# Kernel optimization log

Hardware: AMD Instinct MI355X
Metric: run time of the kernel (lower is better)

The kernel has to match this reference:

```python
import jax, jax.numpy as jnp
import numpy as np

EMBED = 768
HEADS = 12
HEAD_DIM = EMBED // HEADS
B, S = 2, 2048


def setup_inputs() -> dict:
    key = jax.random.key(0)
    ks = jax.random.split(key, 5)
    scale = 1.0 / np.sqrt(EMBED)
    return {
        "x": jax.random.normal(ks[0], (B, S, EMBED), dtype=jnp.float32),
        "w_q": jax.random.normal(ks[1], (EMBED, EMBED), dtype=jnp.float32) * scale,
        "b_q": jnp.zeros((EMBED,), dtype=jnp.float32),
        "w_k": jax.random.normal(ks[2], (EMBED, EMBED), dtype=jnp.float32) * scale,
        "b_k": jnp.zeros((EMBED,), dtype=jnp.float32),
        "w_v": jax.random.normal(ks[3], (EMBED, EMBED), dtype=jnp.float32) * scale,
        "b_v": jnp.zeros((EMBED,), dtype=jnp.float32),
        "w_o": jax.random.normal(ks[4], (EMBED, EMBED), dtype=jnp.float32) * scale,
        "b_o": jnp.zeros((EMBED,), dtype=jnp.float32),
    }


def reference(x, w_q, b_q, w_k, b_k, w_v, b_v, w_o, b_o):
    b, s, _ = x.shape
    # QKV projections (torch Linear: y = x @ W^T + b)
    q = x @ w_q.T + b_q
    k = x @ w_k.T + b_k
    v = x @ w_v.T + b_v
    # split heads -> [b, h, s, d]
    def split(t):
        return t.reshape(b, s, HEADS, HEAD_DIM).transpose(0, 2, 1, 3)
    q, k, v = split(q), split(k), split(v)
    scores = jnp.einsum("bhqd,bhkd->bhqk", q, k) / jnp.sqrt(
        jnp.asarray(HEAD_DIM, dtype=jnp.float32))
    probs = jax.nn.softmax(scores, axis=-1)
    out = jnp.einsum("bhqk,bhkd->bhqd", probs, v)
    out = out.transpose(0, 2, 1, 3).reshape(b, s, EMBED)
    return out @ w_o.T + b_o
```

## Files before the change

kernel.cpp:

```cpp
#include <hip/hip_runtime.h>
#include <math.h>

#define EMBED 768
#define HEADS 12
#define HDIM 64
#define BATCH 2
#define SEQ 2048
#define MTOT (BATCH*SEQ)

typedef short s8v __attribute__((ext_vector_type(8)));
typedef short s4v __attribute__((ext_vector_type(4)));
typedef float f4v __attribute__((ext_vector_type(4)));

__device__ __forceinline__ short f2bf(float f) {
    union { float f; unsigned u; } v; v.f = f;
    unsigned r = v.u + 0x7FFFu + ((v.u >> 16) & 1u);
    return (short)(r >> 16);
}

__device__ __forceinline__ unsigned pk2bf(float a, float b) {
    union { float f; unsigned u; } x, y; x.f = a; y.f = b;
    return ((y.u + 0x8000u) & 0xFFFF0000u) | ((x.u + 0x8000u) >> 16);
}

__device__ __forceinline__ unsigned cvtpk(float a, float b) {
    unsigned r;
    asm("v_cvt_pk_bf16_f32 %0, %1, %2" : "=v"(r) : "v"(a), "v"(b));
    return r;
}

__device__ __forceinline__ float fexp2(float x) {
#if __has_builtin(__builtin_amdgcn_exp2f)
    return __builtin_amdgcn_exp2f(x);
#else
    return exp2f(x);
#endif
}

__device__ __forceinline__ void gll16(const short* g, short* l) {
    __builtin_amdgcn_global_load_lds((const __attribute__((address_space(1))) void*)g,
                                     (__attribute__((address_space(3))) void*)l, 16, 0, 0);
}

__global__ __launch_bounds__(256) void cvt_all(
        const float* __restrict__ x,  const float* __restrict__ wq,
        const float* __restrict__ wk, const float* __restrict__ wv,
        const float* __restrict__ wo,
        short* __restrict__ xb, short* __restrict__ wqb, short* __restrict__ wkb,
        short* __restrict__ wvb, short* __restrict__ wob) {
    const int seg = blockIdx.y;
    const float* src; short* dst; int n4;
    if      (seg == 0) { src = x;  dst = xb;  n4 = MTOT * EMBED / 4; }
    else if (seg == 1) { src = wq; dst = wqb; n4 = EMBED * EMBED / 4; }
    else if (seg == 2) { src = wk; dst = wkb; n4 = EMBED * EMBED / 4; }
    else if (seg == 3) { src = wv; dst = wvb; n4 = EMBED * EMBED / 4; }
    else               { src = wo; dst = wob; n4 = EMBED * EMBED / 4; }
    for (int i = blockIdx.x * 256 + threadIdx.x; i < n4; i += gridDim.x * 256) {
        float4 f = ((const float4*)src)[i];
        short4 o;
        o.x = f2bf(f.x); o.y = f2bf(f.y); o.z = f2bf(f.z); o.w = f2bf(f.w);
        ((short4*)dst)[i] = o;
    }
}

__global__ __launch_bounds__(256, 4) void gemm_qkv(const short* __restrict__ A,
        const short* __restrict__ Wq, const short* __restrict__ Wk, const short* __restrict__ Wv,
        const float* __restrict__ bq, const float* __restrict__ bk, const float* __restrict__ bv,
        short* __restrict__ Qo, short* __restrict__ Ko, short* __restrict__ Vo) {
    const int mode = blockIdx.z;
    const short* W    = (mode == 0) ? Wq : (mode == 1) ? Wk : Wv;
    const float* bias = (mode == 0) ? bq : (mode == 1) ? bk : bv;
    const float qs = (mode == 0) ? (0.125f * 1.44269504f) : 1.0f;

    __shared__ short As[128 * 32];
    __shared__ short Ws[128 * 32];

    const int tid = threadIdx.x;
    const int lane = tid & 63, wid = tid >> 6;
    const int quad = lane >> 4, lr = lane & 15;
    const int m0 = blockIdx.x * 128, n0 = blockIdx.y * 128;
    const int wm = (wid >> 1) * 64, wn = (wid & 1) * 64;
    const int ar = lane >> 2, ac = (lane & 3) * 8;

    f4v acc[4][4];
    for (int a = 0; a < 4; a++)
        for (int b = 0; b < 4; b++)
            for (int i = 0; i < 4; i++) acc[a][b][i] = 0.f;

    for (int k0 = 0; k0 < EMBED; k0 += 32) {
        gll16(&A[(long)(m0 + wid * 32 + ar) * EMBED + k0 + ac],      &As[(wid * 32) * 32]);
        gll16(&A[(long)(m0 + wid * 32 + 16 + ar) * EMBED + k0 + ac], &As[(wid * 32 + 16) * 32]);
        gll16(&W[(long)(n0 + wid * 32 + ar) * EMBED + k0 + ac],      &Ws[(wid * 32) * 32]);
        gll16(&W[(long)(n0 + wid * 32 + 16 + ar) * EMBED + k0 + ac], &Ws[(wid * 32 + 16) * 32]);
        __syncthreads();

        s8v af[4], bf[4];
        for (int mi = 0; mi < 4; mi++)
            af[mi] = *(const s8v*)&As[(wm + mi * 16 + lr) * 32 + quad * 8];
        for (int ni = 0; ni < 4; ni++)
            bf[ni] = *(const s8v*)&Ws[(wn + ni * 16 + lr) * 32 + quad * 8];
        for (int mi = 0; mi < 4; mi++)
            for (int ni = 0; ni < 4; ni++)
                acc[mi][ni] = __builtin_amdgcn_mfma_f32_16x16x32_bf16(af[mi], bf[ni], acc[mi][ni], 0, 0, 0);
        __syncthreads();
    }

    if (mode == 2) {
        for (int mi = 0; mi < 4; mi++) {
            int srow = m0 + wm + mi * 16 + quad * 4;
            int b = srow >> 11, s = srow & 2047;
            for (int ni = 0; ni < 4; ni++) {
                int n = n0 + wn + ni * 16 + lr;
                int h = n >> 6, d = n & 63;
                float bb = bias[n];
                uint2 pk;
                pk.x = pk2bf(acc[mi][ni][0] + bb, acc[mi][ni][1] + bb);
                pk.y = pk2bf(acc[mi][ni][2] + bb, acc[mi][ni][3] + bb);
                *(uint2*)&Vo[(((long)(b * HEADS + h) * HDIM + d) * SEQ) + s] = pk;
            }
        }
    } else {
        short* Out = (mode == 0) ? Qo : Ko;
        for (int mi = 0; mi < 4; mi++) {
            for (int ni = 0; ni < 4; ni++) {
                int n = n0 + wn + ni * 16 + lr;
                int h = n >> 6, d = n & 63;
                float bb = bias[n];
                for (int i = 0; i < 4; i++) {
                    int m = m0 + wm + mi * 16 + quad * 4 + i;
                    int b = m >> 11, s = m & 2047;
                    Out[(((long)(b * HEADS + h) * SEQ + s) * HDIM) + d] =
                        f2bf((acc[mi][ni][i] + bb) * qs);
                }
            }
        }
    }
}

__global__ __launch_bounds__(256, 4) void gemm_out(const short* __restrict__ A,
        const short* __restrict__ W, const float* __restrict__ bias,
        float* __restrict__ Out) {
    __shared__ short As[128 * 32];
    __shared__ short Ws[64 * 32];

    const int tid = threadIdx.x;
    const int lane = tid & 63, wid = tid >> 6;
    const int quad = lane >> 4, lr = lane & 15;
    const int m0 = blockIdx.x * 128, n0 = blockIdx.y * 64;
    const int wm = (wid >> 1) * 64, wn = (wid & 1) * 32;
    const int ar = lane >> 2, ac = (lane & 3) * 8;

    f4v acc[4][2];
    for (int a = 0; a < 4; a++)
        for (int b = 0; b < 2; b++)
            for (int i = 0; i < 4; i++) acc[a][b][i] = 0.f;

    for (int k0 = 0; k0 < EMBED; k0 += 32) {
        gll16(&A[(long)(m0 + wid * 32 + ar) * EMBED + k0 + ac],      &As[(wid * 32) * 32]);
        gll16(&A[(long)(m0 + wid * 32 + 16 + ar) * EMBED + k0 + ac], &As[(wid * 32 + 16) * 32]);
        gll16(&W[(long)(n0 + wid * 16 + ar) * EMBED + k0 + ac],      &Ws[(wid * 16) * 32]);
        __syncthreads();

        s8v af[4], bf[2];
        for (int mi = 0; mi < 4; mi++)
            af[mi] = *(const s8v*)&As[(wm + mi * 16 + lr) * 32 + quad * 8];
        for (int ni = 0; ni < 2; ni++)
            bf[ni] = *(const s8v*)&Ws[(wn + ni * 16 + lr) * 32 + quad * 8];
        for (int mi = 0; mi < 4; mi++)
            for (int ni = 0; ni < 2; ni++)
                acc[mi][ni] = __builtin_amdgcn_mfma_f32_16x16x32_bf16(af[mi], bf[ni], acc[mi][ni], 0, 0, 0);
        __syncthreads();
    }

    for (int mi = 0; mi < 4; mi++)
        for (int ni = 0; ni < 2; ni++)
            for (int i = 0; i < 4; i++) {
                int m = m0 + wm + mi * 16 + quad * 4 + i;
                int n = n0 + wn + ni * 16 + lr;
                Out[(long)m * EMBED + n] = acc[mi][ni][i] + bias[n];
            }
}

__global__ __launch_bounds__(256, 4) void flash_attn(const short* __restrict__ Q,
        const short* __restrict__ K, const short* __restrict__ Vt,
        short* __restrict__ Out) {
    extern __shared__ char pool[];
    short* Ks = (short*)pool;
    short* Vs = Ks + 2 * 64 * 64;

    const int bh = blockIdx.y;
    const int tid = threadIdx.x, lane = tid & 63, wid = tid >> 6;
    const int quad = lane >> 4, lr = lane & 15;
    const int q0 = blockIdx.x * 64;
    const int qw = q0 + wid * 16;

    const short* Qb = Q  + (long)bh * SEQ * HDIM;
    const short* Kb = K  + (long)bh * SEQ * HDIM;
    const short* Vb = Vt + (long)bh * HDIM * SEQ;

    s8v qf[2];
#pragma unroll
    for (int hh = 0; hh < 2; hh++)
        qf[hh] = *(const s8v*)&Qb[(qw + lr) * HDIM + hh * 32 + quad * 8];

    f4v o[4];
#pragma unroll
    for (int dt = 0; dt < 4; dt++)
        for (int i = 0; i < 4; i++) o[dt][i] = 0.f;
    float lsum = 0.f;

    const float SB2 = -16.0f * 1.44269504f;

    const int srow  = lane >> 3;
    const int sslot = (lane & 7) ^ srow;

#pragma unroll
    for (int i = 0; i < 2; i++) {
        const int r0 = wid * 16 + i * 8;
        gll16(&Kb[(long)(r0 + srow) * HDIM + sslot * 8], &Ks[r0 * 64]);
        gll16(&Vb[(long)(r0 + srow) * SEQ + sslot * 8], &Vs[r0 * 64]);
    }
    __syncthreads();

    for (int r = 0; r < 32; r++) {
        const int cur = r & 1;
        const short* Kc = Ks + cur * (64 * 64);
        const short* Vc = Vs + cur * (64 * 64);
        short* Kn = Ks + (cur ^ 1) * (64 * 64);
        short* Vn = Vs + (cur ^ 1) * (64 * 64);

        if (r < 31) {
            const int kn0 = (r + 1) * 64;
#pragma unroll
            for (int i = 0; i < 2; i++) {
                const int r0 = wid * 16 + i * 8;
                gll16(&Kb[(long)(kn0 + r0 + srow) * HDIM + sslot * 8], &Kn[r0 * 64]);
                gll16(&Vb[(long)(r0 + srow) * SEQ + kn0 + sslot * 8], &Vn[r0 * 64]);
            }
        }

        unsigned pw[2][4];
#pragma unroll
        for (int nt = 0; nt < 4; nt++) {
            const int row = nt * 16 + lr;
            s8v kf0 = *(const s8v*)&Kc[row * 64 + ((quad ^ (lr & 7)) * 8)];
            s8v kf1 = *(const s8v*)&Kc[row * 64 + (((4 + quad) ^ (lr & 7)) * 8)];
            f4v s = {SB2, SB2, SB2, SB2};
            s = __builtin_amdgcn_mfma_f32_16x16x32_bf16(kf0, qf[0], s, 0, 0, 0);
            s = __builtin_amdgcn_mfma_f32_16x16x32_bf16(kf1, qf[1], s, 0, 0, 0);
            float p0 = fexp2(s[0]);
            float p1 = fexp2(s[1]);
            float p2 = fexp2(s[2]);
            float p3 = fexp2(s[3]);
            lsum += (p0 + p1) + (p2 + p3);
            pw[nt >> 1][(nt & 1) * 2]     = cvtpk(p0, p1);
            pw[nt >> 1][(nt & 1) * 2 + 1] = cvtpk(p2, p3);
        }

#pragma unroll
        for (int h = 0; h < 2; h++) {
            s8v pf = *(s8v*)&pw[h][0];
            const int cb0 = h * 4 + (quad >> 1);
#pragma unroll
            for (int dt = 0; dt < 4; dt++) {
                const int d = dt * 16 + lr;
                const int c0 = cb0 ^ (lr & 7);
                const int c1 = (cb0 + 2) ^ (lr & 7);
                s4v v0 = *(const s4v*)&Vc[d * 64 + c0 * 8 + (quad & 1) * 4];
                s4v v1 = *(const s4v*)&Vc[d * 64 + c1 * 8 + (quad & 1) * 4];
                s8v vf = __builtin_shufflevector(v0, v1, 0, 1, 2, 3, 4, 5, 6, 7);
                o[dt] = __builtin_amdgcn_mfma_f32_16x16x32_bf16(pf, vf, o[dt], 0, 0, 0);
            }
        }
        __syncthreads();
    }

    lsum += __shfl_xor(lsum, 16);
    lsum += __shfl_xor(lsum, 32);
    float linv[4];
#pragma unroll
    for (int i = 0; i < 4; i++)
        linv[i] = 1.0f / __shfl(lsum, quad * 4 + i);

    const int b = bh / HEADS, h = bh % HEADS;
#pragma unroll
    for (int dt = 0; dt < 4; dt++)
#pragma unroll
        for (int i = 0; i < 4; i++) {
            const int q = qw + quad * 4 + i;
            Out[((long)(b * SEQ + q)) * EMBED + h * HDIM + dt * 16 + lr] =
                f2bf(o[dt][i] * linv[i]);
        }
}

extern "C" void kernel_launch(void* const* d_in, const int* in_sizes, int n_in,
                              void* d_out, int out_size, void* d_ws, size_t ws_size,
                              hipStream_t stream) {
    const float* x   = (const float*)d_in[0];
    const float* w_q = (const float*)d_in[1];
    const float* b_q = (const float*)d_in[2];
    const float* w_k = (const float*)d_in[3];
    const float* b_k = (const float*)d_in[4];
    const float* w_v = (const float*)d_in[5];
    const float* b_v = (const float*)d_in[6];
    const float* w_o = (const float*)d_in[7];
    const float* b_o = (const float*)d_in[8];

    short* x_bf   = (short*)d_ws;
    short* wq_bf  = x_bf  + MTOT * EMBED;
    short* wk_bf  = wq_bf + EMBED * EMBED;
    short* wv_bf  = wk_bf + EMBED * EMBED;
    short* wo_bf  = wv_bf + EMBED * EMBED;
    short* q_bf   = wo_bf + EMBED * EMBED;
    short* k_bf   = q_bf  + BATCH * HEADS * SEQ * HDIM;
    short* v_bf   = k_bf  + BATCH * HEADS * SEQ * HDIM;
    short* att_bf = v_bf  + BATCH * HEADS * SEQ * HDIM;

    cvt_all<<<dim3(1024, 5), 256, 0, stream>>>(x, w_q, w_k, w_v, w_o,
                                               x_bf, wq_bf, wk_bf, wv_bf, wo_bf);

    gemm_qkv<<<dim3(MTOT / 128, EMBED / 128, 3), 256, 0, stream>>>(
        x_bf, wq_bf, wk_bf, wv_bf, b_q, b_k, b_v, q_bf, k_bf, v_bf);

    flash_attn<<<dim3(SEQ / 64, BATCH * HEADS), 256, 32768, stream>>>(
        q_bf, k_bf, v_bf, att_bf);

    gemm_out<<<dim3(MTOT / 128, EMBED / 64), 256, 0, stream>>>(
        att_bf, wo_bf, b_o, (float*)d_out);
}
```

Measured before the change: 164.1 us.

## Widen GEMM K-tile to 64 with XOR-swizzled LDS layout

Both projection GEMMs now stage K-tiles of 64 instead of 32, which halves the number of barrier pairs per output tile. Each 64-element shared-memory row is written with an XOR swizzle on its 16-byte slots, and the MFMA fragment reads apply the same swizzle to avoid LDS bank conflicts. This doubles LDS use per block, which may limit occupancy under the four-blocks-per-CU launch bound.

```diff
diff --git a/kernel.cpp b/kernel.cpp
--- a/kernel.cpp
+++ b/kernel.cpp
@@ -72,43 +72,50 @@
     const float* bias = (mode == 0) ? bq : (mode == 1) ? bk : bv;
     const float qs = (mode == 0) ? (0.125f * 1.44269504f) : 1.0f;
 
-    __shared__ short As[128 * 32];
-    __shared__ short Ws[128 * 32];
+    __shared__ short As[128 * 64];
+    __shared__ short Ws[128 * 64];
 
     const int tid = threadIdx.x;
     const int lane = tid & 63, wid = tid >> 6;
     const int quad = lane >> 4, lr = lane & 15;
     const int m0 = blockIdx.x * 128, n0 = blockIdx.y * 128;
     const int wm = (wid >> 1) * 64, wn = (wid & 1) * 64;
-    const int ar = lane >> 2, ac = (lane & 3) * 8;
+
+    const int srow  = lane >> 3;
+    const int sslot = (lane & 7) ^ srow;
 
     f4v acc[4][4];
     for (int a = 0; a < 4; a++)
         for (int b = 0; b < 4; b++)
             for (int i = 0; i < 4; i++) acc[a][b][i] = 0.f;
 
-    for (int k0 = 0; k0 < EMBED; k0 += 32) {
-        gll16(&A[(long)(m0 + wid * 32 + ar) * EMBED + k0 + ac],      &As[(wid * 32) * 32]);
-        gll16(&A[(long)(m0 + wid * 32 + 16 + ar) * EMBED + k0 + ac], &As[(wid * 32 + 16) * 32]);
-        gll16(&W[(long)(n0 + wid * 32 + ar) * EMBED + k0 + ac],      &Ws[(wid * 32) * 32]);
-        gll16(&W[(long)(n0 + wid * 32 + 16 + ar) * EMBED + k0 + ac], &Ws[(wid * 32 + 16) * 32]);
-        __syncthreads();
-
-        s8v af[4], bf[4];
-        for (int mi = 0; mi < 4; mi++)
-            af[mi] = *(const s8v*)&As[(wm + mi * 16 + lr) * 32 + quad * 8];
-        for (int ni = 0; ni < 4; ni++)
-            bf[ni] = *(const s8v*)&Ws[(wn + ni * 16 + lr) * 32 + quad * 8];
-        for (int mi = 0; mi < 4; mi++)
+    for (int k0 = 0; k0 < EMBED; k0 += 64) {
+#pragma unroll
+        for (int i = 0; i < 4; i++) {
+            const int r0 = wid * 32 + i * 8;
+            gll16(&A[(long)(m0 + r0 + srow) * EMBED + k0 + sslot * 8], &As[r0 * 64]);
+            gll16(&W[(long)(n0 + r0 + srow) * EMBED + k0 + sslot * 8], &Ws[r0 * 64]);
+        }
+        __syncthreads();
+
+#pragma unroll
+        for (int kk = 0; kk < 2; kk++) {
+            s8v af[4], bf[4];
+            for (int mi = 0; mi < 4; mi++)
+                af[mi] = *(const s8v*)&As[(wm + mi * 16 + lr) * 64 + (((kk * 4 + quad) ^ (lr & 7)) * 8)];
             for (int ni = 0; ni < 4; ni++)
-                acc[mi][ni] = __builtin_amdgcn_mfma_f32_16x16x32_bf16(af[mi], bf[ni], acc[mi][ni], 0, 0, 0);
+                bf[ni] = *(const s8v*)&Ws[(wn + ni * 16 + lr) * 64 + (((kk * 4 + quad) ^ (lr & 7)) * 8)];
+            for (int mi = 0; mi < 4; mi++)
+                for (int ni = 0; ni < 4; ni++)
+                    acc[mi][ni] = __builtin_amdgcn_mfma_f32_16x16x32_bf16(af[mi], bf[ni], acc[mi][ni], 0, 0, 0);
+        }
         __syncthreads();
     }
 
     if (mode == 2) {
         for (int mi = 0; mi < 4; mi++) {
-            int srow = m0 + wm + mi * 16 + quad * 4;
-            int b = srow >> 11, s = srow & 2047;
+            int srow2 = m0 + wm + mi * 16 + quad * 4;
+            int b = srow2 >> 11, s = srow2 & 2047;
             for (int ni = 0; ni < 4; ni++) {
                 int n = n0 + wn + ni * 16 + lr;
                 int h = n >> 6, d = n & 63;
@@ -140,35 +147,47 @@
 __global__ __launch_bounds__(256, 4) void gemm_out(const short* __restrict__ A,
         const short* __restrict__ W, const float* __restrict__ bias,
         float* __restrict__ Out) {
-    __shared__ short As[128 * 32];
-    __shared__ short Ws[64 * 32];
+    __shared__ short As[128 * 64];
+    __shared__ short Ws[64 * 64];
 
     const int tid = threadIdx.x;
     const int lane = tid & 63, wid = tid >> 6;
     const int quad = lane >> 4, lr = lane & 15;
     const int m0 = blockIdx.x * 128, n0 = blockIdx.y * 64;
     const int wm = (wid >> 1) * 64, wn = (wid & 1) * 32;
-    const int ar = lane >> 2, ac = (lane & 3) * 8;
+
+    const int srow  = lane >> 3;
+    const int sslot = (lane & 7) ^ srow;
 
     f4v acc[4][2];
     for (int a = 0; a < 4; a++)
         for (int b = 0; b < 2; b++)
             for (int i = 0; i < 4; i++) acc[a][b][i] = 0.f;
 
-    for (int k0 = 0; k0 < EMBED; k0 += 32) {
-        gll16(&A[(long)(m0 + wid * 32 + ar) * EMBED + k0 + ac],      &As[(wid * 32) * 32]);
-        gll16(&A[(long)(m0 + wid * 32 + 16 + ar) * EMBED + k0 + ac], &As[(wid * 32 + 16) * 32]);
-        gll16(&W[(long)(n0 + wid * 16 + ar) * EMBED + k0 + ac],      &Ws[(wid * 16) * 32]);
-        __syncthreads();
-
-        s8v af[4], bf[2];
-        for (int mi = 0; mi < 4; mi++)
-            af[mi] = *(const s8v*)&As[(wm + mi * 16 + lr) * 32 + quad * 8];
-        for (int ni = 0; ni < 2; ni++)
-            bf[ni] = *(const s8v*)&Ws[(wn + ni * 16 + lr) * 32 + quad * 8];
-        for (int mi = 0; mi < 4; mi++)
+    for (int k0 = 0; k0 < EMBED; k0 += 64) {
+#pragma unroll
+        for (int i = 0; i < 4; i++) {
+            const int r0 = wid * 32 + i * 8;
+            gll16(&A[(long)(m0 + r0 + srow) * EMBED + k0 + sslot * 8], &As[r0 * 64]);
+        }
+#pragma unroll
+        for (int i = 0; i < 2; i++) {
+            const int r0 = wid * 16 + i * 8;
+            gll16(&W[(long)(n0 + r0 + srow) * EMBED + k0 + sslot * 8], &Ws[r0 * 64]);
+        }
+        __syncthreads();
+
+#pragma unroll
+        for (int kk = 0; kk < 2; kk++) {
+            s8v af[4], bf[2];
+            for (int mi = 0; mi < 4; mi++)
+                af[mi] = *(const s8v*)&As[(wm + mi * 16 + lr) * 64 + (((kk * 4 + quad) ^ (lr & 7)) * 8)];
             for (int ni = 0; ni < 2; ni++)
-                acc[mi][ni] = __builtin_amdgcn_mfma_f32_16x16x32_bf16(af[mi], bf[ni], acc[mi][ni], 0, 0, 0);
+                bf[ni] = *(const s8v*)&Ws[(wn + ni * 16 + lr) * 64 + (((kk * 4 + quad) ^ (lr & 7)) * 8)];
+            for (int mi = 0; mi < 4; mi++)
+                for (int ni = 0; ni < 2; ni++)
+                    acc[mi][ni] = __builtin_amdgcn_mfma_f32_16x16x32_bf16(af[mi], bf[ni], acc[mi][ni], 0, 0, 0);
+        }
         __syncthreads();
     }
 
```

New measurement: 155.7 us. -5.1%, faster.

## Triple-buffer LDS loads in QKV and output GEMMs with async prefetch

Applied to the files above, without the earlier changes.

Both projection GEMMs now use a three-stage LDS ring buffer. Direct global-to-LDS loads are issued two k-steps ahead, with manual vmcnt waits and one barrier per iteration replacing the two __syncthreads. The goal is to hide global memory latency behind MFMA work. The cost is triple the shared memory and a lower occupancy hint (3 blocks instead of 4) on gemm_qkv.

```diff
diff --git a/kernel.cpp b/kernel.cpp
--- a/kernel.cpp
+++ b/kernel.cpp
@@ -63,7 +63,7 @@
     }
 }
 
-__global__ __launch_bounds__(256, 4) void gemm_qkv(const short* __restrict__ A,
+__global__ __launch_bounds__(256, 3) void gemm_qkv(const short* __restrict__ A,
         const short* __restrict__ Wq, const short* __restrict__ Wk, const short* __restrict__ Wv,
         const float* __restrict__ bq, const float* __restrict__ bk, const float* __restrict__ bv,
         short* __restrict__ Qo, short* __restrict__ Ko, short* __restrict__ Vo) {
@@ -72,8 +72,8 @@
     const float* bias = (mode == 0) ? bq : (mode == 1) ? bk : bv;
     const float qs = (mode == 0) ? (0.125f * 1.44269504f) : 1.0f;
 
-    __shared__ short As[128 * 32];
-    __shared__ short Ws[128 * 32];
+    __shared__ short As[3][128 * 32];
+    __shared__ short Ws[3][128 * 32];
 
     const int tid = threadIdx.x;
     const int lane = tid & 63, wid = tid >> 6;
@@ -87,28 +87,56 @@
         for (int b = 0; b < 4; b++)
             for (int i = 0; i < 4; i++) acc[a][b][i] = 0.f;
 
-    for (int k0 = 0; k0 < EMBED; k0 += 32) {
-        gll16(&A[(long)(m0 + wid * 32 + ar) * EMBED + k0 + ac],      &As[(wid * 32) * 32]);
-        gll16(&A[(long)(m0 + wid * 32 + 16 + ar) * EMBED + k0 + ac], &As[(wid * 32 + 16) * 32]);
-        gll16(&W[(long)(n0 + wid * 32 + ar) * EMBED + k0 + ac],      &Ws[(wid * 32) * 32]);
-        gll16(&W[(long)(n0 + wid * 32 + 16 + ar) * EMBED + k0 + ac], &Ws[(wid * 32 + 16) * 32]);
-        __syncthreads();
+    gll16(&A[(long)(m0 + wid * 32 + ar) * EMBED + ac],      &As[0][(wid * 32) * 32]);
+    gll16(&A[(long)(m0 + wid * 32 + 16 + ar) * EMBED + ac], &As[0][(wid * 32 + 16) * 32]);
+    gll16(&W[(long)(n0 + wid * 32 + ar) * EMBED + ac],      &Ws[0][(wid * 32) * 32]);
+    gll16(&W[(long)(n0 + wid * 32 + 16 + ar) * EMBED + ac], &Ws[0][(wid * 32 + 16) * 32]);
+    __builtin_amdgcn_sched_barrier(0);
+    gll16(&A[(long)(m0 + wid * 32 + ar) * EMBED + 32 + ac],      &As[1][(wid * 32) * 32]);
+    gll16(&A[(long)(m0 + wid * 32 + 16 + ar) * EMBED + 32 + ac], &As[1][(wid * 32 + 16) * 32]);
+    gll16(&W[(long)(n0 + wid * 32 + ar) * EMBED + 32 + ac],      &Ws[1][(wid * 32) * 32]);
+    gll16(&W[(long)(n0 + wid * 32 + 16 + ar) * EMBED + 32 + ac], &Ws[1][(wid * 32 + 16) * 32]);
+    __builtin_amdgcn_sched_barrier(0);
+    asm volatile("s_waitcnt vmcnt(4)" ::: "memory");
+    __builtin_amdgcn_s_barrier();
+    __builtin_amdgcn_sched_barrier(0);
+
+    int cur = 0;
+    for (int t = 0; t < 24; t++) {
+        if (t < 22) {
+            const int nx = (cur >= 1) ? (cur - 1) : 2;
+            const int kn = (t + 2) * 32;
+            gll16(&A[(long)(m0 + wid * 32 + ar) * EMBED + kn + ac],      &As[nx][(wid * 32) * 32]);
+            gll16(&A[(long)(m0 + wid * 32 + 16 + ar) * EMBED + kn + ac], &As[nx][(wid * 32 + 16) * 32]);
+            gll16(&W[(long)(n0 + wid * 32 + ar) * EMBED + kn + ac],      &Ws[nx][(wid * 32) * 32]);
+            gll16(&W[(long)(n0 + wid * 32 + 16 + ar) * EMBED + kn + ac], &Ws[nx][(wid * 32 + 16) * 32]);
+        }
+        __builtin_amdgcn_sched_barrier(0);
 
         s8v af[4], bf[4];
+#pragma unroll
         for (int mi = 0; mi < 4; mi++)
-            af[mi] = *(const s8v*)&As[(wm + mi * 16 + lr) * 32 + quad * 8];
+            af[mi] = *(const s8v*)&As[cur][(wm + mi * 16 + lr) * 32 + quad * 8];
+#pragma unroll
         for (int ni = 0; ni < 4; ni++)
-            bf[ni] = *(const s8v*)&Ws[(wn + ni * 16 + lr) * 32 + quad * 8];
+            bf[ni] = *(const s8v*)&Ws[cur][(wn + ni * 16 + lr) * 32 + quad * 8];
+#pragma unroll
         for (int mi = 0; mi < 4; mi++)
+#pragma unroll
             for (int ni = 0; ni < 4; ni++)
                 acc[mi][ni] = __builtin_amdgcn_mfma_f32_16x16x32_bf16(af[mi], bf[ni], acc[mi][ni], 0, 0, 0);
-        __syncthreads();
+
+        if (t < 22) { asm volatile("s_waitcnt vmcnt(4)" ::: "memory"); }
+        else        { asm volatile("s_waitcnt vmcnt(0)" ::: "memory"); }
+        __builtin_amdgcn_s_barrier();
+        __builtin_amdgcn_sched_barrier(0);
+        cur = (cur == 2) ? 0 : cur + 1;
     }
 
     if (mode == 2) {
         for (int mi = 0; mi < 4; mi++) {
-            int srow = m0 + wm + mi * 16 + quad * 4;
-            int b = srow >> 11, s = srow & 2047;
+            int srow2 = m0 + wm + mi * 16 + quad * 4;
+            int b = srow2 >> 11, s = srow2 & 2047;
             for (int ni = 0; ni < 4; ni++) {
                 int n = n0 + wn + ni * 16 + lr;
                 int h = n >> 6, d = n & 63;
@@ -140,8 +168,8 @@
 __global__ __launch_bounds__(256, 4) void gemm_out(const short* __restrict__ A,
         const short* __restrict__ W, const float* __restrict__ bias,
         float* __restrict__ Out) {
-    __shared__ short As[128 * 32];
-    __shared__ short Ws[64 * 32];
+    __shared__ short As[3][128 * 32];
+    __shared__ short Ws[3][64 * 32];
 
     const int tid = threadIdx.x;
     const int lane = tid & 63, wid = tid >> 6;
@@ -155,21 +183,47 @@
         for (int b = 0; b < 2; b++)
             for (int i = 0; i < 4; i++) acc[a][b][i] = 0.f;
 
-    for (int k0 = 0; k0 < EMBED; k0 += 32) {
-        gll16(&A[(long)(m0 + wid * 32 + ar) * EMBED + k0 + ac],      &As[(wid * 32) * 32]);
-        gll16(&A[(long)(m0 + wid * 32 + 16 + ar) * EMBED + k0 + ac], &As[(wid * 32 + 16) * 32]);
-        gll16(&W[(long)(n0 + wid * 16 + ar) * EMBED + k0 + ac],      &Ws[(wid * 16) * 32]);
-        __syncthreads();
+    gll16(&A[(long)(m0 + wid * 32 + ar) * EMBED + ac],      &As[0][(wid * 32) * 32]);
+    gll16(&A[(long)(m0 + wid * 32 + 16 + ar) * EMBED + ac], &As[0][(wid * 32 + 16) * 32]);
+    gll16(&W[(long)(n0 + wid * 16 + ar) * EMBED + ac],      &Ws[0][(wid * 16) * 32]);
+    __builtin_amdgcn_sched_barrier(0);
+    gll16(&A[(long)(m0 + wid * 32 + ar) * EMBED + 32 + ac],      &As[1][(wid * 32) * 32]);
+    gll16(&A[(long)(m0 + wid * 32 + 16 + ar) * EMBED + 32 + ac], &As[1][(wid * 32 + 16) * 32]);
+    gll16(&W[(long)(n0 + wid * 16 + ar) * EMBED + 32 + ac],      &Ws[1][(wid * 16) * 32]);
+    __builtin_amdgcn_sched_barrier(0);
+    asm volatile("s_waitcnt vmcnt(3)" ::: "memory");
+    __builtin_amdgcn_s_barrier();
+    __builtin_amdgcn_sched_barrier(0);
+
+    int cur = 0;
+    for (int t = 0; t < 24; t++) {
+        if (t < 22) {
+            const int nx = (cur >= 1) ? (cur - 1) : 2;
+            const int kn = (t + 2) * 32;
+            gll16(&A[(long)(m0 + wid * 32 + ar) * EMBED + kn + ac],      &As[nx][(wid * 32) * 32]);
+            gll16(&A[(long)(m0 + wid * 32 + 16 + ar) * EMBED + kn + ac], &As[nx][(wid * 32 + 16) * 32]);
+            gll16(&W[(long)(n0 + wid * 16 + ar) * EMBED + kn + ac],      &Ws[nx][(wid * 16) * 32]);
+        }
+        __builtin_amdgcn_sched_barrier(0);
 
         s8v af[4], bf[2];
+#pragma unroll
         for (int mi = 0; mi < 4; mi++)
-            af[mi] = *(const s8v*)&As[(wm + mi * 16 + lr) * 32 + quad * 8];
+            af[mi] = *(const s8v*)&As[cur][(wm + mi * 16 + lr) * 32 + quad * 8];
+#pragma unroll
         for (int ni = 0; ni < 2; ni++)
-            bf[ni] = *(const s8v*)&Ws[(wn + ni * 16 + lr) * 32 + quad * 8];
+            bf[ni] = *(const s8v*)&Ws[cur][(wn + ni * 16 + lr) * 32 + quad * 8];
+#pragma unroll
         for (int mi = 0; mi < 4; mi++)
+#pragma unroll
             for (int ni = 0; ni < 2; ni++)
                 acc[mi][ni] = __builtin_amdgcn_mfma_f32_16x16x32_bf16(af[mi], bf[ni], acc[mi][ni], 0, 0, 0);
-        __syncthreads();
+
+        if (t < 22) { asm volatile("s_waitcnt vmcnt(3)" ::: "memory"); }
+        else        { asm volatile("s_waitcnt vmcnt(0)" ::: "memory"); }
+        __builtin_amdgcn_s_barrier();
+        __builtin_amdgcn_sched_barrier(0);
+        cur = (cur == 2) ? 0 : cur + 1;
     }
 
     for (int mi = 0; mi < 4; mi++)
```

Measured after the change: 162.0 us. About the same (-1.3%).
